# Performance work log

Measured on AMD Instinct MI355X. Metric: run time of the kernel, lower is better.

## Reference

```python
import jax, jax.numpy as jnp
import numpy as np

DIM = 1024
HIDDEN = 2816  # multiple_of * ceil(int(2*4096/3)/multiple_of)
N_MODALITIES = 2
B, S = 8, 4096


def setup_inputs() -> dict:
    key = jax.random.key(0)
    k_x, k_m, k1, k2, k3 = jax.random.split(key, 5)
    x = jax.random.normal(k_x, (B, S, DIM), dtype=jnp.float32)
    modality_ids = jax.random.randint(k_m, (B, S), 0, N_MODALITIES, dtype=jnp.int32)
    in_std = DIM ** -0.5
    out_std = HIDDEN ** -0.5
    # Linear weight layout: [out_features, in_features], stacked over modalities.
    W1 = jax.random.normal(k1, (N_MODALITIES, HIDDEN, DIM), dtype=jnp.float32) * in_std
    W3 = jax.random.normal(k3, (N_MODALITIES, HIDDEN, DIM), dtype=jnp.float32) * in_std
    W2 = jax.random.normal(k2, (N_MODALITIES, DIM, HIDDEN), dtype=jnp.float32) * out_std
    return {"x": x, "modality_ids": modality_ids, "W1": W1, "W2": W2, "W3": W3}


def reference(x, modality_ids, W1, W2, W3):
    # Masked per-modality SwiGLU; equivalent to gather -> expert MLP -> scatter.
    output = jnp.zeros_like(x)
    for m in range(N_MODALITIES):  # small fixed modality count
        mask = (modality_ids == m)[..., None]          # [B, S, 1]
        x1 = jnp.einsum('bsd,hd->bsh', x, W1[m])       # gate proj
        x3 = jnp.einsum('bsd,hd->bsh', x, W3[m])       # up proj
        out_m = jnp.einsum('bsh,dh->bsd', jax.nn.silu(x1) * x3, W2[m])
        output = output + jnp.where(mask, out_m, 0.0)
    return output
```

## Files before the change

### kernel.cpp

```cpp
#include <hip/hip_runtime.h>
#include <stdint.h>

#define DIMK 1024
#define HID  2816

typedef __attribute__((ext_vector_type(8))) __bf16 bf16x8;
typedef __attribute__((ext_vector_type(4))) float  f32x4;

typedef const __attribute__((address_space(1))) void* gas1_t;
typedef __attribute__((address_space(3))) void*       las3_t;

__device__ __forceinline__ uint16_t f2bf(float f) {
  uint32_t u = __float_as_uint(f);
  u += 0x7FFFu + ((u >> 16) & 1u);
  return (uint16_t)(u >> 16);
}

__device__ __forceinline__ void gload16(const uint16_t* g, uint16_t* l) {
  __builtin_amdgcn_global_load_lds((gas1_t)g, (las3_t)l, 16, 0, 0);
}

template<int N> __device__ __forceinline__ void wait_vm() {
  if constexpr (N == 0)      asm volatile("s_waitcnt vmcnt(0)" ::: "memory");
  else if constexpr (N == 2) asm volatile("s_waitcnt vmcnt(2)" ::: "memory");
  else if constexpr (N == 4) asm volatile("s_waitcnt vmcnt(4)" ::: "memory");
  else                       asm volatile("s_waitcnt vmcnt(6)" ::: "memory");
}

__device__ __forceinline__ void stage_half(const uint16_t* g, long stride,
                                           uint16_t* lds, int wv, int lane) {
  const int rsub = lane >> 3;
  const int gsw  = ((lane & 7) ^ rsub) << 3;
#pragma unroll
  for (int j = 0; j < 2; ++j) {
    const int blk = j * 8 + wv;
    gload16(g + (long)(blk * 8 + rsub) * stride + gsw,
            lds + blk * 512 + lane * 8);
  }
}

__device__ __forceinline__ bf16x8 ldsf(const uint16_t* lds, int r, int g) {
  return *reinterpret_cast<const bf16x8*>(lds + r * 64 + ((g ^ (r & 7)) << 3));
}


__global__ void count_kernel(const int* __restrict__ mids, int* __restrict__ bc, int T) {
  const int b = blockIdx.x, t = threadIdx.x;
  const int token = b * 256 + t;
  const int lane = t & 63, wv = t >> 6;
  const int m = (token < T) ? mids[token] : -1;
  unsigned long long m0 = __ballot(m == 0);
  unsigned long long m1 = __ballot(m == 1);
  __shared__ int w0[4], w1[4];
  if (lane == 0) { w0[wv] = __popcll(m0); w1[wv] = __popcll(m1); }
  __syncthreads();
  if (t == 0) {
    bc[2 * b]     = w0[0] + w0[1] + w0[2] + w0[3];
    bc[2 * b + 1] = w1[0] + w1[1] + w1[2] + w1[3];
  }
}

__global__ void scan_kernel(const int* __restrict__ bc, int* __restrict__ base,
                            int* __restrict__ counters, int nb) {
  __shared__ int s0[256], s1[256];
  const int t = threadIdx.x;
  const int v0 = (t < nb) ? bc[2 * t] : 0;
  const int v1 = (t < nb) ? bc[2 * t + 1] : 0;
  s0[t] = v0; s1[t] = v1;
  __syncthreads();
  for (int off = 1; off < 256; off <<= 1) {
    int a0 = (t >= off) ? s0[t - off] : 0;
    int a1 = (t >= off) ? s1[t - off] : 0;
    __syncthreads();
    s0[t] += a0; s1[t] += a1;
    __syncthreads();
  }
  if (t < nb) { base[2 * t] = s0[t] - v0; base[2 * t + 1] = s1[t] - v1; }
  if (t == nb - 1) { counters[0] = s0[t]; counters[1] = s1[t]; }
}

__global__ void slot_kernel(const int* __restrict__ mids, const int* __restrict__ base,
                            const int* __restrict__ counters, int* __restrict__ tok,
                            int* __restrict__ slotof, int T) {
  const int b = blockIdx.x, t = threadIdx.x;
  const int token = b * 256 + t;
  const int lane = t & 63, wv = t >> 6;
  const int m = (token < T) ? mids[token] : -1;
  unsigned long long m0 = __ballot(m == 0);
  unsigned long long m1 = __ballot(m == 1);
  __shared__ int w0[4], w1[4];
  if (lane == 0) { w0[wv] = __popcll(m0); w1[wv] = __popcll(m1); }
  __syncthreads();
  int pre0 = 0, pre1 = 0;
  for (int w = 0; w < wv; ++w) { pre0 += w0[w]; pre1 += w1[w]; }
  if (token >= T) return;
  const unsigned long long below = (1ULL << lane) - 1ULL;
  const int c0 = counters[0];
  const int al0 = ((c0 + 255) >> 8) << 8;
  int slot;
  if (m == 0) slot = base[2 * b] + pre0 + __popcll(m0 & below);
  else        slot = al0 + base[2 * b + 1] + pre1 + __popcll(m1 & below);
  tok[slot] = token;
  slotof[token] = slot;
}

__global__ void copy_kernel(const float* __restrict__ x, const int* __restrict__ slotof,
                            uint16_t* __restrict__ xg, int T) {
  const int token = blockIdx.x * 4 + (threadIdx.x >> 6);
  if (token >= T) return;
  const int lane = threadIdx.x & 63;
  const int slot = slotof[token];
  const float4* src = (const float4*)(x + (long)token * DIMK);
  uint16_t* dst = xg + (long)slot * DIMK;
#pragma unroll
  for (int j = 0; j < 4; ++j) {
    float4 v = src[lane + 64 * j];
    ushort4 o;
    o.x = f2bf(v.x); o.y = f2bf(v.y); o.z = f2bf(v.z); o.w = f2bf(v.w);
    *(ushort4*)(dst + (lane + 64 * j) * 4) = o;
  }
}

__global__ void convert_kernel(const float* __restrict__ src, uint16_t* __restrict__ dst, long n) {
  long i = ((long)blockIdx.x * blockDim.x + threadIdx.x) * 4;
  if (i >= n) return;
  float4 v = *(const float4*)(src + i);
  ushort4 o;
  o.x = f2bf(v.x); o.y = f2bf(v.y); o.z = f2bf(v.z); o.w = f2bf(v.w);
  *(ushort4*)(dst + i) = o;
}


template<bool PF, int W0, int W1, int W2>
__device__ __forceinline__ void quad_tile(
    const uint16_t* Ac, const uint16_t* Bxc, const uint16_t* Byc,
    uint16_t* An, uint16_t* Bxn, uint16_t* Byn,
    const uint16_t* gA, const uint16_t* gBx, const uint16_t* gBy,
    long ko, long stride,
    int wv, int lane, int wr, int wc, int lrow, int grp,
    f32x4 (&accX)[8][2], f32x4 (&accY)[8][2]) {
  bf16x8 a[4][2], bx[2][2], by[2][2];
  wait_vm<W0>();
  __builtin_amdgcn_s_barrier();
  asm volatile("" ::: "memory");
#pragma unroll
  for (int m = 0; m < 4; ++m) {
    a[m][0] = ldsf(Ac, m * 32 + wr * 16 + lrow, grp);
    a[m][1] = ldsf(Ac, m * 32 + wr * 16 + lrow, 4 + grp);
  }
#pragma unroll
  for (int n = 0; n < 2; ++n) {
    bx[n][0] = ldsf(Bxc, wc * 32 + n * 16 + lrow, grp);
    bx[n][1] = ldsf(Bxc, wc * 32 + n * 16 + lrow, 4 + grp);
  }
  if constexpr (PF) stage_half(gA + ko, stride, An, wv, lane);
  asm volatile("s_waitcnt lgkmcnt(0)" ::: "memory");
  __builtin_amdgcn_sched_barrier(0);
  __builtin_amdgcn_s_setprio(1);
#pragma unroll
  for (int ks = 0; ks < 2; ++ks)
#pragma unroll
    for (int m = 0; m < 4; ++m)
#pragma unroll
      for (int n = 0; n < 2; ++n)
        accX[m][n] = __builtin_amdgcn_mfma_f32_16x16x32_bf16(a[m][ks], bx[n][ks], accX[m][n], 0, 0, 0);
  __builtin_amdgcn_s_setprio(0);
  wait_vm<W1>();
  __builtin_amdgcn_s_barrier();
  asm volatile("" ::: "memory");
#pragma unroll
  for (int n = 0; n < 2; ++n) {
    by[n][0] = ldsf(Byc, wc * 32 + n * 16 + lrow, grp);
    by[n][1] = ldsf(Byc, wc * 32 + n * 16 + lrow, 4 + grp);
  }
  if constexpr (PF) stage_half(gBx + ko, stride, Bxn, wv, lane);
  asm volatile("s_waitcnt lgkmcnt(0)" ::: "memory");
  __builtin_amdgcn_sched_barrier(0);
  __builtin_amdgcn_s_setprio(1);
#pragma unroll
  for (int ks = 0; ks < 2; ++ks)
#pragma unroll
    for (int m = 0; m < 4; ++m)
#pragma unroll
      for (int n = 0; n < 2; ++n)
        accY[m][n] = __builtin_amdgcn_mfma_f32_16x16x32_bf16(a[m][ks], by[n][ks], accY[m][n], 0, 0, 0);
  __builtin_amdgcn_s_setprio(0);
  wait_vm<W2>();
  __builtin_amdgcn_s_barrier();
  asm volatile("" ::: "memory");
#pragma unroll
  for (int m = 0; m < 4; ++m) {
    a[m][0] = ldsf(Ac, (m + 4) * 32 + wr * 16 + lrow, grp);
    a[m][1] = ldsf(Ac, (m + 4) * 32 + wr * 16 + lrow, 4 + grp);
  }
  if constexpr (PF) stage_half(gBy + ko, stride, Byn, wv, lane);
  asm volatile("s_waitcnt lgkmcnt(0)" ::: "memory");
  __builtin_amdgcn_sched_barrier(0);
  __builtin_amdgcn_s_setprio(1);
#pragma unroll
  for (int ks = 0; ks < 2; ++ks)
#pragma unroll
    for (int m = 0; m < 4; ++m)
#pragma unroll
      for (int n = 0; n < 2; ++n)
        accX[m + 4][n] = __builtin_amdgcn_mfma_f32_16x16x32_bf16(a[m][ks], bx[n][ks], accX[m + 4][n], 0, 0, 0);
  __builtin_amdgcn_s_setprio(0);
  if constexpr (PF) stage_half(gA + 128 * stride + ko, stride, An + 128 * 64, wv, lane);
  __builtin_amdgcn_s_setprio(1);
#pragma unroll
  for (int ks = 0; ks < 2; ++ks)
#pragma unroll
    for (int m = 0; m < 4; ++m)
#pragma unroll
      for (int n = 0; n < 2; ++n)
        accY[m + 4][n] = __builtin_amdgcn_mfma_f32_16x16x32_bf16(a[m][ks], by[n][ks], accY[m + 4][n], 0, 0, 0);
  __builtin_amdgcn_s_setprio(0);
}


__global__ __launch_bounds__(512, 2) void gemm1_kernel(
    const uint16_t* __restrict__ xg, const uint16_t* __restrict__ w1b,
    const uint16_t* __restrict__ w3b, uint16_t* __restrict__ hbuf,
    const int* __restrict__ counters) {
  __shared__ __align__(16) uint16_t lsA[2][256 * 64];
  __shared__ __align__(16) uint16_t lsB1[2][128 * 64];
  __shared__ __align__(16) uint16_t lsB3[2][128 * 64];

  const int c0 = counters[0], c1 = counters[1];
  const int t0 = (c0 + 255) >> 8, t1 = (c1 + 255) >> 8;
  const int GX = gridDim.x;
  const int nwg = GX * (int)gridDim.y;
  const int orig = blockIdx.y * GX + blockIdx.x;
  const int q = nwg >> 3, r = nwg & 7;
  const int xcd = orig & 7, loc = orig >> 3;
  const int swz = (xcd < r ? xcd * (q + 1) : r * (q + 1) + (xcd - r) * q) + loc;
  const int ht = swz / GX;
  const int rt = swz - ht * GX;
  if (rt >= t0 + t1) return;
  const int mod = (rt < t0) ? 0 : 1;
  const long row0 = (long)rt * 256;

  const int tid = threadIdx.x, lane = tid & 63, wv = tid >> 6;
  const int wr = wv >> 2, wc = wv & 3;
  const int lrow = lane & 15, grp = lane >> 4;

  const uint16_t* gA  = xg  + row0 * DIMK;
  const uint16_t* gB1 = w1b + ((long)mod * HID + ht * 128) * DIMK;
  const uint16_t* gB3 = w3b + ((long)mod * HID + ht * 128) * DIMK;

  f32x4 accG[8][2], accU[8][2];
#pragma unroll
  for (int m = 0; m < 8; ++m)
#pragma unroll
    for (int n = 0; n < 2; ++n) {
      accG[m][n] = {0.f, 0.f, 0.f, 0.f};
      accU[m][n] = {0.f, 0.f, 0.f, 0.f};
    }

  stage_half(gA,              DIMK, &lsA[0][0],         wv, lane);
  stage_half(gB1,             DIMK, &lsB1[0][0],        wv, lane);
  stage_half(gB3,             DIMK, &lsB3[0][0],        wv, lane);
  stage_half(gA + 128 * DIMK, DIMK, &lsA[0][128 * 64],  wv, lane);

  const int NT = DIMK / 64;
  int cur = 0;
  for (int t = 0; t < NT - 1; ++t) {
    quad_tile<true, 4, 4, 4>(&lsA[cur][0], &lsB1[cur][0], &lsB3[cur][0],
                             &lsA[cur ^ 1][0], &lsB1[cur ^ 1][0], &lsB3[cur ^ 1][0],
                             gA, gB1, gB3, (long)(t + 1) * 64, DIMK,
                             wv, lane, wr, wc, lrow, grp, accG, accU);
    cur ^= 1;
  }
  quad_tile<false, 4, 2, 0>(&lsA[cur][0], &lsB1[cur][0], &lsB3[cur][0],
                            &lsA[cur ^ 1][0], &lsB1[cur ^ 1][0], &lsB3[cur ^ 1][0],
                            gA, gB1, gB3, 0, DIMK,
                            wv, lane, wr, wc, lrow, grp, accG, accU);

#pragma unroll
  for (int m = 0; m < 8; ++m)
#pragma unroll
    for (int n = 0; n < 2; ++n) {
      const int col = ht * 128 + wc * 32 + n * 16 + lrow;
#pragma unroll
      for (int i = 0; i < 4; ++i) {
        const long row = row0 + m * 32 + wr * 16 + grp * 4 + i;
        float g = accG[m][n][i];
        float u = accU[m][n][i];
        float hv = (g / (1.f + __expf(-g))) * u;
        hbuf[row * HID + col] = f2bf(hv);
      }
    }
}


__global__ __launch_bounds__(512, 2) void gemm2_kernel(
    const uint16_t* __restrict__ hbuf, const uint16_t* __restrict__ w2b,
    const int* __restrict__ counters, const int* __restrict__ tok,
    float* __restrict__ out) {
  __shared__ __align__(16) uint16_t lsA[2][256 * 64];
  __shared__ __align__(16) uint16_t lsBx[2][128 * 64];
  __shared__ __align__(16) uint16_t lsBy[2][128 * 64];

  const int c0 = counters[0], c1 = counters[1];
  const int t0 = (c0 + 255) >> 8, t1 = (c1 + 255) >> 8;
  const int NCT = gridDim.y;
  const int nwg = gridDim.x * NCT;
  const int orig = blockIdx.y * gridDim.x + blockIdx.x;
  const int q = nwg >> 3, r = nwg & 7;
  const int xcd = orig & 7, loc = orig >> 3;
  const int swz = (xcd < r ? xcd * (q + 1) : r * (q + 1) + (xcd - r) * q) + loc;
  const int rt = swz / NCT;
  const int ct = swz - rt * NCT;
  if (rt >= t0 + t1) return;
  const int mod = (rt < t0) ? 0 : 1;
  const long row0 = (long)rt * 256;
  const int vlimit = (mod == 0) ? c0 : t0 * 256 + c1;

  const int tid = threadIdx.x, lane = tid & 63, wv = tid >> 6;
  const int wr = wv >> 2, wc = wv & 3;
  const int lrow = lane & 15, grp = lane >> 4;

  const uint16_t* gA  = hbuf + row0 * HID;
  const uint16_t* gBx = w2b + ((long)mod * DIMK + ct * 256) * HID;
  const uint16_t* gBy = gBx + 128 * HID;

  f32x4 accX[8][2], accY[8][2];
#pragma unroll
  for (int m = 0; m < 8; ++m)
#pragma unroll
    for (int n = 0; n < 2; ++n) {
      accX[m][n] = {0.f, 0.f, 0.f, 0.f};
      accY[m][n] = {0.f, 0.f, 0.f, 0.f};
    }

  stage_half(gA,             HID, &lsA[0][0],        wv, lane);
  stage_half(gBx,            HID, &lsBx[0][0],       wv, lane);
  stage_half(gBy,            HID, &lsBy[0][0],       wv, lane);
  stage_half(gA + 128 * HID, HID, &lsA[0][128 * 64], wv, lane);

  const int NT = HID / 64;
  int cur = 0;
  for (int t = 0; t < NT - 1; ++t) {
    quad_tile<true, 4, 4, 4>(&lsA[cur][0], &lsBx[cur][0], &lsBy[cur][0],
                             &lsA[cur ^ 1][0], &lsBx[cur ^ 1][0], &lsBy[cur ^ 1][0],
                             gA, gBx, gBy, (long)(t + 1) * 64, HID,
                             wv, lane, wr, wc, lrow, grp, accX, accY);
    cur ^= 1;
  }
  quad_tile<false, 4, 2, 0>(&lsA[cur][0], &lsBx[cur][0], &lsBy[cur][0],
                            &lsA[cur ^ 1][0], &lsBx[cur ^ 1][0], &lsBy[cur ^ 1][0],
                            gA, gBx, gBy, 0, HID,
                            wv, lane, wr, wc, lrow, grp, accX, accY);

#pragma unroll
  for (int m = 0; m < 8; ++m)
#pragma unroll
    for (int n = 0; n < 2; ++n) {
      const int colX = ct * 256 + wc * 32 + n * 16 + lrow;
#pragma unroll
      for (int i = 0; i < 4; ++i) {
        const int row = (int)row0 + m * 32 + wr * 16 + grp * 4 + i;
        if (row < vlimit) {
          const long obase = (long)tok[row] * DIMK;
          out[obase + colX]       = accX[m][n][i];
          out[obase + colX + 128] = accY[m][n][i];
        }
      }
    }
}

extern "C" void kernel_launch(void* const* d_in, const int* in_sizes, int n_in,
                              void* d_out, int out_size, void* d_ws, size_t ws_size,
                              hipStream_t stream) {
  const float* x    = (const float*)d_in[0];
  const int*   mids = (const int*)d_in[1];
  const float* W1   = (const float*)d_in[2];
  const float* W2   = (const float*)d_in[3];
  const float* W3   = (const float*)d_in[4];
  float* out = (float*)d_out;

  const int T   = in_sizes[1];
  const int NB  = (T + 255) / 256;
  const int CAP = ((T + 255) & ~255) + 256;

  char* ws = (char*)d_ws;
  int* counters = (int*)ws;
  int* bc   = (int*)(ws + 256);
  int* base = (int*)(ws + 256 + 2048);
  int* tok  = (int*)(ws + 256 + 4096);
  int* slotof = tok + ((CAP + 63) & ~63);
  size_t off = 256 + 4096 + (size_t)((CAP + 63) & ~63) * 4 + (size_t)((T + 63) & ~63) * 4;
  off = (off + 255) & ~(size_t)255;
  uint16_t* xg  = (uint16_t*)(ws + off); off += (size_t)CAP * DIMK * 2;
  uint16_t* w1b = (uint16_t*)(ws + off); off += (size_t)2 * HID * DIMK * 2;
  uint16_t* w3b = (uint16_t*)(ws + off); off += (size_t)2 * HID * DIMK * 2;
  uint16_t* w2b = (uint16_t*)(ws + off); off += (size_t)2 * DIMK * HID * 2;
  uint16_t* hbuf = (uint16_t*)(ws + off); off += (size_t)CAP * HID * 2;
  (void)ws_size; (void)n_in; (void)out_size;

  count_kernel<<<NB, 256, 0, stream>>>(mids, bc, T);
  scan_kernel<<<1, 256, 0, stream>>>(bc, base, counters, NB);
  slot_kernel<<<NB, 256, 0, stream>>>(mids, base, counters, tok, slotof, T);
  copy_kernel<<<(T + 3) / 4, 256, 0, stream>>>(x, slotof, xg, T);

  const long NW = (long)2 * HID * DIMK;
  const int cblk = (int)((NW / 4 + 255) / 256);
  convert_kernel<<<cblk, 256, 0, stream>>>(W1, w1b, NW);
  convert_kernel<<<cblk, 256, 0, stream>>>(W3, w3b, NW);
  convert_kernel<<<cblk, 256, 0, stream>>>(W2, w2b, NW);

  const int rtiles = CAP / 256;
  gemm1_kernel<<<dim3(rtiles, HID / 128), 512, 0, stream>>>(xg, w1b, w3b, hbuf, counters);
  gemm2_kernel<<<dim3(rtiles, DIMK / 256), 512, 0, stream>>>(hbuf, w2b, counters, tok, out);
}
```

Baseline: 706.1 us.

## Shrink GEMM tiles to 128 rows and K-step 32 for higher occupancy

Both grouped GEMMs move from 256-row tiles with a K-step of 64 to 128-row tiles with a K-step of 32. This cuts LDS and accumulator registers so that four workgroups can fit per CU, raising launch bounds from 2 to 4. The slot alignment, capacity and grid swizzle mapping are changed to match 128-row tiles, and the three weight-conversion launches are merged into one. The cost is lower data reuse per tile, twice as many K iterations with barriers, and a shallower prefetch pipeline.

```diff
diff --git a/kernel.cpp b/kernel.cpp
--- a/kernel.cpp
+++ b/kernel.cpp
@@ -22,25 +22,19 @@
 
 template<int N> __device__ __forceinline__ void wait_vm() {
   if constexpr (N == 0)      asm volatile("s_waitcnt vmcnt(0)" ::: "memory");
+  else if constexpr (N == 1) asm volatile("s_waitcnt vmcnt(1)" ::: "memory");
   else if constexpr (N == 2) asm volatile("s_waitcnt vmcnt(2)" ::: "memory");
-  else if constexpr (N == 4) asm volatile("s_waitcnt vmcnt(4)" ::: "memory");
-  else                       asm volatile("s_waitcnt vmcnt(6)" ::: "memory");
-}
-
-__device__ __forceinline__ void stage_half(const uint16_t* g, long stride,
-                                           uint16_t* lds, int wv, int lane) {
-  const int rsub = lane >> 3;
-  const int gsw  = ((lane & 7) ^ rsub) << 3;
-#pragma unroll
-  for (int j = 0; j < 2; ++j) {
-    const int blk = j * 8 + wv;
-    gload16(g + (long)(blk * 8 + rsub) * stride + gsw,
-            lds + blk * 512 + lane * 8);
-  }
-}
-
-__device__ __forceinline__ bf16x8 ldsf(const uint16_t* lds, int r, int g) {
-  return *reinterpret_cast<const bf16x8*>(lds + r * 64 + ((g ^ (r & 7)) << 3));
+}
+
+__device__ __forceinline__ void stage32(const uint16_t* g, long stride,
+                                        uint16_t* lds, int tid) {
+  const int row  = tid >> 2;
+  const int srcg = (tid & 3) ^ ((tid >> 3) & 3);
+  gload16(g + (long)row * stride + srcg * 8, lds + tid * 8);
+}
+
+__device__ __forceinline__ bf16x8 ldsf32(const uint16_t* lds, int r, int g) {
+  return *reinterpret_cast<const bf16x8*>(lds + r * 32 + ((g ^ ((r >> 1) & 3)) << 3));
 }
 
 
@@ -96,7 +90,7 @@
   if (token >= T) return;
   const unsigned long long below = (1ULL << lane) - 1ULL;
   const int c0 = counters[0];
-  const int al0 = ((c0 + 255) >> 8) << 8;
+  const int al0 = ((c0 + 127) >> 7) << 7;
   int slot;
   if (m == 0) slot = base[2 * b] + pre0 + __popcll(m0 & below);
   else        slot = al0 + base[2 * b + 1] + pre1 + __popcll(m1 & below);
@@ -121,8 +115,15 @@
   }
 }
 
-__global__ void convert_kernel(const float* __restrict__ src, uint16_t* __restrict__ dst, long n) {
-  long i = ((long)blockIdx.x * blockDim.x + threadIdx.x) * 4;
+__global__ void convert3_kernel(const float* __restrict__ s0, const float* __restrict__ s1,
+                                const float* __restrict__ s2, uint16_t* __restrict__ d0,
+                                uint16_t* __restrict__ d1, uint16_t* __restrict__ d2,
+                                long n, int cblk) {
+  const int seg = blockIdx.x / cblk;
+  const int bid = blockIdx.x - seg * cblk;
+  const float* src = (seg == 0) ? s0 : (seg == 1) ? s1 : s2;
+  uint16_t*    dst = (seg == 0) ? d0 : (seg == 1) ? d1 : d2;
+  long i = ((long)bid * blockDim.x + threadIdx.x) * 4;
   if (i >= n) return;
   float4 v = *(const float4*)(src + i);
   ushort4 o;
@@ -131,114 +132,77 @@
 }
 
 
-template<bool PF, int W0, int W1, int W2>
-__device__ __forceinline__ void quad_tile(
+template<bool PF, int W0, int W1>
+__device__ __forceinline__ void qt32(
     const uint16_t* Ac, const uint16_t* Bxc, const uint16_t* Byc,
     uint16_t* An, uint16_t* Bxn, uint16_t* Byn,
     const uint16_t* gA, const uint16_t* gBx, const uint16_t* gBy,
     long ko, long stride,
-    int wv, int lane, int wr, int wc, int lrow, int grp,
-    f32x4 (&accX)[8][2], f32x4 (&accY)[8][2]) {
-  bf16x8 a[4][2], bx[2][2], by[2][2];
+    int tid, int wr, int wc, int lrow, int grp,
+    f32x4 (&accX)[4][2], f32x4 (&accY)[4][2]) {
+  bf16x8 a[4], bx[2], by[2];
   wait_vm<W0>();
   __builtin_amdgcn_s_barrier();
   asm volatile("" ::: "memory");
 #pragma unroll
-  for (int m = 0; m < 4; ++m) {
-    a[m][0] = ldsf(Ac, m * 32 + wr * 16 + lrow, grp);
-    a[m][1] = ldsf(Ac, m * 32 + wr * 16 + lrow, 4 + grp);
-  }
-#pragma unroll
-  for (int n = 0; n < 2; ++n) {
-    bx[n][0] = ldsf(Bxc, wc * 32 + n * 16 + lrow, grp);
-    bx[n][1] = ldsf(Bxc, wc * 32 + n * 16 + lrow, 4 + grp);
-  }
-  if constexpr (PF) stage_half(gA + ko, stride, An, wv, lane);
+  for (int m = 0; m < 4; ++m)
+    a[m] = ldsf32(Ac, wr * 64 + m * 16 + lrow, grp);
+#pragma unroll
+  for (int n = 0; n < 2; ++n)
+    bx[n] = ldsf32(Bxc, wc * 32 + n * 16 + lrow, grp);
+  if constexpr (PF) stage32(gA + ko, stride, An, tid);
   asm volatile("s_waitcnt lgkmcnt(0)" ::: "memory");
   __builtin_amdgcn_sched_barrier(0);
   __builtin_amdgcn_s_setprio(1);
 #pragma unroll
-  for (int ks = 0; ks < 2; ++ks)
-#pragma unroll
-    for (int m = 0; m < 4; ++m)
-#pragma unroll
-      for (int n = 0; n < 2; ++n)
-        accX[m][n] = __builtin_amdgcn_mfma_f32_16x16x32_bf16(a[m][ks], bx[n][ks], accX[m][n], 0, 0, 0);
+  for (int m = 0; m < 4; ++m)
+#pragma unroll
+    for (int n = 0; n < 2; ++n)
+      accX[m][n] = __builtin_amdgcn_mfma_f32_16x16x32_bf16(a[m], bx[n], accX[m][n], 0, 0, 0);
   __builtin_amdgcn_s_setprio(0);
   wait_vm<W1>();
   __builtin_amdgcn_s_barrier();
   asm volatile("" ::: "memory");
 #pragma unroll
-  for (int n = 0; n < 2; ++n) {
-    by[n][0] = ldsf(Byc, wc * 32 + n * 16 + lrow, grp);
-    by[n][1] = ldsf(Byc, wc * 32 + n * 16 + lrow, 4 + grp);
-  }
-  if constexpr (PF) stage_half(gBx + ko, stride, Bxn, wv, lane);
+  for (int n = 0; n < 2; ++n)
+    by[n] = ldsf32(Byc, wc * 32 + n * 16 + lrow, grp);
+  if constexpr (PF) {
+    stage32(gBx + ko, stride, Bxn, tid);
+    stage32(gBy + ko, stride, Byn, tid);
+  }
   asm volatile("s_waitcnt lgkmcnt(0)" ::: "memory");
   __builtin_amdgcn_sched_barrier(0);
   __builtin_amdgcn_s_setprio(1);
 #pragma unroll
-  for (int ks = 0; ks < 2; ++ks)
-#pragma unroll
-    for (int m = 0; m < 4; ++m)
-#pragma unroll
-      for (int n = 0; n < 2; ++n)
-        accY[m][n] = __builtin_amdgcn_mfma_f32_16x16x32_bf16(a[m][ks], by[n][ks], accY[m][n], 0, 0, 0);
+  for (int m = 0; m < 4; ++m)
+#pragma unroll
+    for (int n = 0; n < 2; ++n)
+      accY[m][n] = __builtin_amdgcn_mfma_f32_16x16x32_bf16(a[m], by[n], accY[m][n], 0, 0, 0);
   __builtin_amdgcn_s_setprio(0);
-  wait_vm<W2>();
-  __builtin_amdgcn_s_barrier();
-  asm volatile("" ::: "memory");
-#pragma unroll
-  for (int m = 0; m < 4; ++m) {
-    a[m][0] = ldsf(Ac, (m + 4) * 32 + wr * 16 + lrow, grp);
-    a[m][1] = ldsf(Ac, (m + 4) * 32 + wr * 16 + lrow, 4 + grp);
-  }
-  if constexpr (PF) stage_half(gBy + ko, stride, Byn, wv, lane);
-  asm volatile("s_waitcnt lgkmcnt(0)" ::: "memory");
-  __builtin_amdgcn_sched_barrier(0);
-  __builtin_amdgcn_s_setprio(1);
-#pragma unroll
-  for (int ks = 0; ks < 2; ++ks)
-#pragma unroll
-    for (int m = 0; m < 4; ++m)
-#pragma unroll
-      for (int n = 0; n < 2; ++n)
-        accX[m + 4][n] = __builtin_amdgcn_mfma_f32_16x16x32_bf16(a[m][ks], bx[n][ks], accX[m + 4][n], 0, 0, 0);
-  __builtin_amdgcn_s_setprio(0);
-  if constexpr (PF) stage_half(gA + 128 * stride + ko, stride, An + 128 * 64, wv, lane);
-  __builtin_amdgcn_s_setprio(1);
-#pragma unroll
-  for (int ks = 0; ks < 2; ++ks)
-#pragma unroll
-    for (int m = 0; m < 4; ++m)
-#pragma unroll
-      for (int n = 0; n < 2; ++n)
-        accY[m + 4][n] = __builtin_amdgcn_mfma_f32_16x16x32_bf16(a[m][ks], by[n][ks], accY[m + 4][n], 0, 0, 0);
-  __builtin_amdgcn_s_setprio(0);
-}
-
-
-__global__ __launch_bounds__(512, 2) void gemm1_kernel(
+}
+
+
+__global__ __launch_bounds__(512, 4) void gemm1_kernel(
     const uint16_t* __restrict__ xg, const uint16_t* __restrict__ w1b,
     const uint16_t* __restrict__ w3b, uint16_t* __restrict__ hbuf,
     const int* __restrict__ counters) {
-  __shared__ __align__(16) uint16_t lsA[2][256 * 64];
-  __shared__ __align__(16) uint16_t lsB1[2][128 * 64];
-  __shared__ __align__(16) uint16_t lsB3[2][128 * 64];
+  __shared__ __align__(16) uint16_t lsA[2][128 * 32];
+  __shared__ __align__(16) uint16_t lsB1[2][128 * 32];
+  __shared__ __align__(16) uint16_t lsB3[2][128 * 32];
 
   const int c0 = counters[0], c1 = counters[1];
-  const int t0 = (c0 + 255) >> 8, t1 = (c1 + 255) >> 8;
-  const int GX = gridDim.x;
-  const int nwg = GX * (int)gridDim.y;
-  const int orig = blockIdx.y * GX + blockIdx.x;
+  const int t0 = (c0 + 127) >> 7, t1 = (c1 + 127) >> 7;
+  const int NHT = gridDim.y;
+  const int nwg = gridDim.x * NHT;
+  const int orig = blockIdx.y * gridDim.x + blockIdx.x;
   const int q = nwg >> 3, r = nwg & 7;
   const int xcd = orig & 7, loc = orig >> 3;
   const int swz = (xcd < r ? xcd * (q + 1) : r * (q + 1) + (xcd - r) * q) + loc;
-  const int ht = swz / GX;
-  const int rt = swz - ht * GX;
+  const int rt = swz / NHT;
+  const int ht = swz - rt * NHT;
   if (rt >= t0 + t1) return;
   const int mod = (rt < t0) ? 0 : 1;
-  const long row0 = (long)rt * 256;
+  const long row0 = (long)rt * 128;
 
   const int tid = threadIdx.x, lane = tid & 63, wv = tid >> 6;
   const int wr = wv >> 2, wc = wv & 3;
@@ -248,42 +212,41 @@
   const uint16_t* gB1 = w1b + ((long)mod * HID + ht * 128) * DIMK;
   const uint16_t* gB3 = w3b + ((long)mod * HID + ht * 128) * DIMK;
 
-  f32x4 accG[8][2], accU[8][2];
-#pragma unroll
-  for (int m = 0; m < 8; ++m)
+  f32x4 accG[4][2], accU[4][2];
+#pragma unroll
+  for (int m = 0; m < 4; ++m)
 #pragma unroll
     for (int n = 0; n < 2; ++n) {
       accG[m][n] = {0.f, 0.f, 0.f, 0.f};
       accU[m][n] = {0.f, 0.f, 0.f, 0.f};
     }
 
-  stage_half(gA,              DIMK, &lsA[0][0],         wv, lane);
-  stage_half(gB1,             DIMK, &lsB1[0][0],        wv, lane);
-  stage_half(gB3,             DIMK, &lsB3[0][0],        wv, lane);
-  stage_half(gA + 128 * DIMK, DIMK, &lsA[0][128 * 64],  wv, lane);
-
-  const int NT = DIMK / 64;
+  stage32(gA,  DIMK, &lsA[0][0],  tid);
+  stage32(gB1, DIMK, &lsB1[0][0], tid);
+  stage32(gB3, DIMK, &lsB3[0][0], tid);
+
+  const int NT = DIMK / 32;
   int cur = 0;
   for (int t = 0; t < NT - 1; ++t) {
-    quad_tile<true, 4, 4, 4>(&lsA[cur][0], &lsB1[cur][0], &lsB3[cur][0],
-                             &lsA[cur ^ 1][0], &lsB1[cur ^ 1][0], &lsB3[cur ^ 1][0],
-                             gA, gB1, gB3, (long)(t + 1) * 64, DIMK,
-                             wv, lane, wr, wc, lrow, grp, accG, accU);
+    qt32<true, 1, 1>(&lsA[cur][0], &lsB1[cur][0], &lsB3[cur][0],
+                     &lsA[cur ^ 1][0], &lsB1[cur ^ 1][0], &lsB3[cur ^ 1][0],
+                     gA, gB1, gB3, (long)(t + 1) * 32, DIMK,
+                     tid, wr, wc, lrow, grp, accG, accU);
     cur ^= 1;
   }
-  quad_tile<false, 4, 2, 0>(&lsA[cur][0], &lsB1[cur][0], &lsB3[cur][0],
-                            &lsA[cur ^ 1][0], &lsB1[cur ^ 1][0], &lsB3[cur ^ 1][0],
-                            gA, gB1, gB3, 0, DIMK,
-                            wv, lane, wr, wc, lrow, grp, accG, accU);
-
-#pragma unroll
-  for (int m = 0; m < 8; ++m)
+  qt32<false, 1, 0>(&lsA[cur][0], &lsB1[cur][0], &lsB3[cur][0],
+                    &lsA[cur ^ 1][0], &lsB1[cur ^ 1][0], &lsB3[cur ^ 1][0],
+                    gA, gB1, gB3, 0, DIMK,
+                    tid, wr, wc, lrow, grp, accG, accU);
+
+#pragma unroll
+  for (int m = 0; m < 4; ++m)
 #pragma unroll
     for (int n = 0; n < 2; ++n) {
       const int col = ht * 128 + wc * 32 + n * 16 + lrow;
 #pragma unroll
       for (int i = 0; i < 4; ++i) {
-        const long row = row0 + m * 32 + wr * 16 + grp * 4 + i;
+        const long row = row0 + wr * 64 + m * 16 + grp * 4 + i;
         float g = accG[m][n][i];
         float u = accU[m][n][i];
         float hv = (g / (1.f + __expf(-g))) * u;
@@ -293,16 +256,16 @@
 }
 
 
-__global__ __launch_bounds__(512, 2) void gemm2_kernel(
+__global__ __launch_bounds__(512, 4) void gemm2_kernel(
     const uint16_t* __restrict__ hbuf, const uint16_t* __restrict__ w2b,
     const int* __restrict__ counters, const int* __restrict__ tok,
     float* __restrict__ out) {
-  __shared__ __align__(16) uint16_t lsA[2][256 * 64];
-  __shared__ __align__(16) uint16_t lsBx[2][128 * 64];
-  __shared__ __align__(16) uint16_t lsBy[2][128 * 64];
+  __shared__ __align__(16) uint16_t lsA[2][128 * 32];
+  __shared__ __align__(16) uint16_t lsBx[2][128 * 32];
+  __shared__ __align__(16) uint16_t lsBy[2][128 * 32];
 
   const int c0 = counters[0], c1 = counters[1];
-  const int t0 = (c0 + 255) >> 8, t1 = (c1 + 255) >> 8;
+  const int t0 = (c0 + 127) >> 7, t1 = (c1 + 127) >> 7;
   const int NCT = gridDim.y;
   const int nwg = gridDim.x * NCT;
   const int orig = blockIdx.y * gridDim.x + blockIdx.x;
@@ -313,8 +276,8 @@
   const int ct = swz - rt * NCT;
   if (rt >= t0 + t1) return;
   const int mod = (rt < t0) ? 0 : 1;
-  const long row0 = (long)rt * 256;
-  const int vlimit = (mod == 0) ? c0 : t0 * 256 + c1;
+  const long row0 = (long)rt * 128;
+  const int vlimit = (mod == 0) ? c0 : t0 * 128 + c1;
 
   const int tid = threadIdx.x, lane = tid & 63, wv = tid >> 6;
   const int wr = wv >> 2, wc = wv & 3;
@@ -324,42 +287,41 @@
   const uint16_t* gBx = w2b + ((long)mod * DIMK + ct * 256) * HID;
   const uint16_t* gBy = gBx + 128 * HID;
 
-  f32x4 accX[8][2], accY[8][2];
-#pragma unroll
-  for (int m = 0; m < 8; ++m)
+  f32x4 accX[4][2], accY[4][2];
+#pragma unroll
+  for (int m = 0; m < 4; ++m)
 #pragma unroll
     for (int n = 0; n < 2; ++n) {
       accX[m][n] = {0.f, 0.f, 0.f, 0.f};
       accY[m][n] = {0.f, 0.f, 0.f, 0.f};
     }
 
-  stage_half(gA,             HID, &lsA[0][0],        wv, lane);
-  stage_half(gBx,            HID, &lsBx[0][0],       wv, lane);
-  stage_half(gBy,            HID, &lsBy[0][0],       wv, lane);
-  stage_half(gA + 128 * HID, HID, &lsA[0][128 * 64], wv, lane);
-
-  const int NT = HID / 64;
+  stage32(gA,  HID, &lsA[0][0],  tid);
+  stage32(gBx, HID, &lsBx[0][0], tid);
+  stage32(gBy, HID, &lsBy[0][0], tid);
+
+  const int NT = HID / 32;
   int cur = 0;
   for (int t = 0; t < NT - 1; ++t) {
-    quad_tile<true, 4, 4, 4>(&lsA[cur][0], &lsBx[cur][0], &lsBy[cur][0],
-                             &lsA[cur ^ 1][0], &lsBx[cur ^ 1][0], &lsBy[cur ^ 1][0],
-                             gA, gBx, gBy, (long)(t + 1) * 64, HID,
-                             wv, lane, wr, wc, lrow, grp, accX, accY);
+    qt32<true, 1, 1>(&lsA[cur][0], &lsBx[cur][0], &lsBy[cur][0],
+                     &lsA[cur ^ 1][0], &lsBx[cur ^ 1][0], &lsBy[cur ^ 1][0],
+                     gA, gBx, gBy, (long)(t + 1) * 32, HID,
+                     tid, wr, wc, lrow, grp, accX, accY);
     cur ^= 1;
   }
-  quad_tile<false, 4, 2, 0>(&lsA[cur][0], &lsBx[cur][0], &lsBy[cur][0],
-                            &lsA[cur ^ 1][0], &lsBx[cur ^ 1][0], &lsBy[cur ^ 1][0],
-                            gA, gBx, gBy, 0, HID,
-                            wv, lane, wr, wc, lrow, grp, accX, accY);
-
-#pragma unroll
-  for (int m = 0; m < 8; ++m)
+  qt32<false, 1, 0>(&lsA[cur][0], &lsBx[cur][0], &lsBy[cur][0],
+                    &lsA[cur ^ 1][0], &lsBx[cur ^ 1][0], &lsBy[cur ^ 1][0],
+                    gA, gBx, gBy, 0, HID,
+                    tid, wr, wc, lrow, grp, accX, accY);
+
+#pragma unroll
+  for (int m = 0; m < 4; ++m)
 #pragma unroll
     for (int n = 0; n < 2; ++n) {
       const int colX = ct * 256 + wc * 32 + n * 16 + lrow;
 #pragma unroll
       for (int i = 0; i < 4; ++i) {
-        const int row = (int)row0 + m * 32 + wr * 16 + grp * 4 + i;
+        const int row = (int)row0 + wr * 64 + m * 16 + grp * 4 + i;
         if (row < vlimit) {
           const long obase = (long)tok[row] * DIMK;
           out[obase + colX]       = accX[m][n][i];
@@ -381,7 +343,7 @@
 
   const int T   = in_sizes[1];
   const int NB  = (T + 255) / 256;
-  const int CAP = ((T + 255) & ~255) + 256;
+  const int CAP = ((T + 127) & ~127) + 128;
 
   char* ws = (char*)d_ws;
   int* counters = (int*)ws;
@@ -405,11 +367,9 @@
 
   const long NW = (long)2 * HID * DIMK;
   const int cblk = (int)((NW / 4 + 255) / 256);
-  convert_kernel<<<cblk, 256, 0, stream>>>(W1, w1b, NW);
-  convert_kernel<<<cblk, 256, 0, stream>>>(W3, w3b, NW);
-  convert_kernel<<<cblk, 256, 0, stream>>>(W2, w2b, NW);
-
-  const int rtiles = CAP / 256;
+  convert3_kernel<<<3 * cblk, 256, 0, stream>>>(W1, W3, W2, w1b, w3b, w2b, NW, cblk);
+
+  const int rtiles = CAP / 128;
   gemm1_kernel<<<dim3(rtiles, HID / 128), 512, 0, stream>>>(xg, w1b, w3b, hbuf, counters);
   gemm2_kernel<<<dim3(rtiles, DIMK / 256), 512, 0, stream>>>(hbuf, w2b, counters, tok, out);
 }
```

Result: slower. 724.6 us (+2.6%).
